# Optimization experiments

Hardware: AMD Instinct MI355X
Metric: run time of the kernel (lower is better)

## Reference

```python
import jax, jax.numpy as jnp
import numpy as np

N_NODES = 100000
N_EDGES = 1600000
IN_FEATS, HIDDEN_FEATS, OUT_FEATS = 32, 64, 16


def setup_inputs() -> dict:
    key = jax.random.key(0)
    ks = jax.random.split(key, 8)
    return {
        "features": jax.random.normal(ks[0], (N_NODES, IN_FEATS), dtype=jnp.float32),
        "src": jax.random.randint(ks[1], (N_EDGES,), 0, N_NODES, dtype=jnp.int64),
        "dst": jax.random.randint(ks[2], (N_EDGES,), 0, N_NODES, dtype=jnp.int64),
        "W1_self": jax.random.normal(ks[3], (IN_FEATS, HIDDEN_FEATS), dtype=jnp.float32) * 0.1,
        "W1_neigh": jax.random.normal(ks[4], (IN_FEATS, HIDDEN_FEATS), dtype=jnp.float32) * 0.1,
        "b1": jnp.zeros((HIDDEN_FEATS,), dtype=jnp.float32),
        "W2_self": jax.random.normal(ks[5], (HIDDEN_FEATS, OUT_FEATS), dtype=jnp.float32) * 0.1,
        "W2_neigh": jax.random.normal(ks[6], (HIDDEN_FEATS, OUT_FEATS), dtype=jnp.float32) * 0.1,
        "b2": jnp.zeros((OUT_FEATS,), dtype=jnp.float32),
    }


def _sage_conv_mean(h, src, dst, n_nodes, W_self, W_neigh, b):
    # DGL SAGEConv(mean): gather src features to edges, mean-reduce at dst,
    # then fc_self(h) + fc_neigh(mean_neigh) + bias.
    ones = jnp.ones(src.shape, dtype=h.dtype)
    deg = jax.ops.segment_sum(ones, dst, num_segments=n_nodes)  # in-degree [N]
    agg = jax.ops.segment_sum(h[src], dst, num_segments=n_nodes)  # [N, d]
    mean_neigh = agg / jnp.maximum(deg, 1.0)[:, None]
    return h @ W_self + mean_neigh @ W_neigh + b


def reference(features, src, dst, W1_self, W1_neigh, b1, W2_self, W2_neigh, b2):
    n = features.shape[0]
    h = _sage_conv_mean(features, src, dst, n, W1_self, W1_neigh, b1)
    h = jax.nn.relu(h)
    # dropout is identity at inference (Keras call default training=False)
    out = _sage_conv_mean(h, src, dst, n, W2_self, W2_neigh, b2)
    return out
```

## Files before the change

### kernel.cpp

```cpp
#include <hip/hip_runtime.h>

#define N_NODES 100000
#define N_EDGES 1600000
#define IN_F 32
#define HID_F 64
#define OUT_F 16
#define BSIZE 512
#define NBKT 256
#define CAP 10240
#define CHUNK 4096
#define NBUCK ((N_NODES + BSIZE - 1) / BSIZE)
#define APITCH 68

__device__ __forceinline__ unsigned f2bf(float f) {
  unsigned u = __float_as_uint(f);
  return (u + 0x7FFFu + ((u >> 16) & 1u)) >> 16;
}

#define ADD8(s, V) do { \
  s[0] += __uint_as_float((V).x << 16); \
  s[1] += __uint_as_float((V).x & 0xFFFF0000u); \
  s[2] += __uint_as_float((V).y << 16); \
  s[3] += __uint_as_float((V).y & 0xFFFF0000u); \
  s[4] += __uint_as_float((V).z << 16); \
  s[5] += __uint_as_float((V).z & 0xFFFF0000u); \
  s[6] += __uint_as_float((V).w << 16); \
  s[7] += __uint_as_float((V).w & 0xFFFF0000u); } while (0)

__global__ __launch_bounds__(256) void f2bf_kernel(
    const float4* __restrict__ in, uint4* __restrict__ outp) {
  int i = blockIdx.x * 256 + threadIdx.x;
  if (i >= N_NODES * IN_F / 8) return;
  float4 a = in[2 * i], b = in[2 * i + 1];
  uint4 r;
  r.x = f2bf(a.x) | (f2bf(a.y) << 16);
  r.y = f2bf(a.z) | (f2bf(a.w) << 16);
  r.z = f2bf(b.x) | (f2bf(b.y) << 16);
  r.w = f2bf(b.z) | (f2bf(b.w) << 16);
  outp[i] = r;
}

__global__ __launch_bounds__(NBKT) void cursor_init_kernel(int* __restrict__ cursor) {
  cursor[threadIdx.x] = threadIdx.x * CAP;
}

__global__ __launch_bounds__(512) void bucket_kernel(
    const int* __restrict__ src, const int* __restrict__ dst,
    int* __restrict__ cursor, unsigned* __restrict__ sorted) {
  __shared__ unsigned stage[CHUNK];
  __shared__ unsigned char sbkt[CHUNK];
  __shared__ int lcnt[NBKT], lscan[NBKT], gbase[NBKT];
  int t = threadIdx.x;
  if (t < NBKT) lcnt[t] = 0;
  __syncthreads();

  int base = blockIdx.x * CHUNK;
  unsigned mypk[CHUNK / 512];
  int myb[CHUNK / 512], myrank[CHUNK / 512];
#pragma unroll
  for (int i = 0; i < CHUNK / 512; ++i) {
    int e = base + t + 512 * i;
    if (e < N_EDGES) {
      unsigned s = (unsigned)src[e], d = (unsigned)dst[e];
      myb[i] = (int)(d >> 9);
      mypk[i] = (s << 9) | (d & 511u);
      myrank[i] = atomicAdd(&lcnt[myb[i]], 1);
    } else {
      myb[i] = -1;
    }
  }
  __syncthreads();
  if (t < NBKT) lscan[t] = lcnt[t];
  __syncthreads();
  for (int off = 1; off < NBKT; off <<= 1) {
    int v = (t < NBKT && t >= off) ? lscan[t - off] : 0;
    __syncthreads();
    if (t < NBKT) lscan[t] += v;
    __syncthreads();
  }
  if (t < NBKT) gbase[t] = lcnt[t] ? atomicAdd(&cursor[t], lcnt[t]) : 0;
  __syncthreads();
#pragma unroll
  for (int i = 0; i < CHUNK / 512; ++i) {
    if (myb[i] >= 0) {
      int slot = (lscan[myb[i]] - lcnt[myb[i]]) + myrank[i];
      stage[slot] = mypk[i];
      sbkt[slot] = (unsigned char)myb[i];
    }
  }
  __syncthreads();
  int nvalid = min(CHUNK, N_EDGES - base);
  for (int i = t; i < nvalid; i += 512) {
    unsigned p = stage[i];
    int b = (int)sbkt[i];
    int addr = gbase[b] + (i - (lscan[b] - lcnt[b]));
    sorted[addr] = p;
  }
}

__global__ __launch_bounds__(1024) void bcsr_kernel(
    const unsigned* __restrict__ sorted, const int* __restrict__ cursor,
    int* __restrict__ ptr, int* __restrict__ col) {
  __shared__ int lcnt[BSIZE];
  __shared__ int lcur[BSIZE];
  __shared__ int scanbuf[BSIZE];
  int t = threadIdx.x;
  int b = blockIdx.x;
  int base = b * CAP;
  int ne = cursor[b] - base;

  if (t < BSIZE) lcnt[t] = 0;
  __syncthreads();
  for (int i = t; i < ne; i += 1024)
    atomicAdd(&lcnt[sorted[base + i] & (BSIZE - 1)], 1);
  __syncthreads();

  int c = 0;
  if (t < BSIZE) { c = lcnt[t]; scanbuf[t] = c; }
  __syncthreads();
  for (int off = 1; off < BSIZE; off <<= 1) {
    int u = (t < BSIZE && t >= off) ? scanbuf[t - off] : 0;
    __syncthreads();
    if (t < BSIZE) scanbuf[t] += u;
    __syncthreads();
  }
  if (t < BSIZE) {
    int incl = scanbuf[t];
    lcur[t] = base + incl - c;
    int v = b * BSIZE + t;
    if (v < N_NODES) ptr[v] = base + incl;
  }
  __syncthreads();

  for (int i = t; i < ne; i += 1024) {
    unsigned p = sorted[base + i];
    int pos = atomicAdd(&lcur[p & (BSIZE - 1)], 1);
    col[pos] = (int)(p >> 9);
  }
}

__global__ __launch_bounds__(256) void gather1_kernel(
    const int* __restrict__ ptr, const int* __restrict__ col,
    const uint4* __restrict__ featbf, float* __restrict__ meanf) {
  int gid = blockIdx.x * 256 + threadIdx.x;
  int v = gid >> 2;
  int c = gid & 3;
  if (v >= N_NODES) return;
  int start = (v & (BSIZE - 1)) ? ptr[v - 1] : (v >> 9) * CAP;
  int end = ptr[v];
  float s[8] = {0.f, 0.f, 0.f, 0.f, 0.f, 0.f, 0.f, 0.f};
  int e = start;
  for (; e + 3 < end; e += 4) {
    uint4 q0 = featbf[col[e] * 4 + c];
    uint4 q1 = featbf[col[e + 1] * 4 + c];
    uint4 q2 = featbf[col[e + 2] * 4 + c];
    uint4 q3 = featbf[col[e + 3] * 4 + c];
    ADD8(s, q0);
    ADD8(s, q1);
    ADD8(s, q2);
    ADD8(s, q3);
  }
  for (; e < end; ++e) {
    uint4 q = featbf[col[e] * 4 + c];
    ADD8(s, q);
  }
  float inv = 1.0f / fmaxf((float)(end - start), 1.0f);
  float4 r0 = {s[0] * inv, s[1] * inv, s[2] * inv, s[3] * inv};
  float4 r1 = {s[4] * inv, s[5] * inv, s[6] * inv, s[7] * inv};
  ((float4*)meanf)[v * 8 + 2 * c] = r0;
  ((float4*)meanf)[v * 8 + 2 * c + 1] = r1;
}

__global__ __launch_bounds__(256) void l1t2s2_kernel(
    const float* __restrict__ feat, const float* __restrict__ meanf,
    const float* __restrict__ W1s, const float* __restrict__ W1n,
    const float* __restrict__ b1,
    const float* __restrict__ W2n, const float* __restrict__ W2s,
    unsigned* __restrict__ t2u, float* __restrict__ s2) {
  __shared__ float sA[64 * APITCH];
  __shared__ float sW[64 * 64];

  int t = threadIdx.x;
  int tile = blockIdx.x * 64;
  int nvalid = min(64, N_NODES - tile);

  {
    const float4* Fg = (const float4*)(feat + (size_t)tile * IN_F);
    const float4* Mg = (const float4*)(meanf + (size_t)tile * IN_F);
    int lim = nvalid * 8;
#pragma unroll
    for (int it = 0; it < 2; ++it) {
      int idx = t + 256 * it;
      int n = idx >> 3, c = idx & 7;
      if (idx < lim) {
        float4 a = Fg[idx];
        sA[(4 * c + 0) * APITCH + n] = a.x;
        sA[(4 * c + 1) * APITCH + n] = a.y;
        sA[(4 * c + 2) * APITCH + n] = a.z;
        sA[(4 * c + 3) * APITCH + n] = a.w;
        float4 m = Mg[idx];
        sA[(32 + 4 * c + 0) * APITCH + n] = m.x;
        sA[(32 + 4 * c + 1) * APITCH + n] = m.y;
        sA[(32 + 4 * c + 2) * APITCH + n] = m.z;
        sA[(32 + 4 * c + 3) * APITCH + n] = m.w;
      }
    }
  }
  {
    float4* Ws = (float4*)sW;
#pragma unroll
    for (int it = 0; it < 4; ++it) {
      int idx = t + 256 * it;
      int row = idx >> 4;
      const float4* srcw = (row < 32) ? (const float4*)W1s : (const float4*)W1n;
      Ws[idx] = srcw[(row & 31) * 16 + (idx & 15)];
    }
  }
  int tx = t & 15, ty = t >> 4;
  int n0 = 4 * ty, c0 = 4 * tx;
  float4 bb = ((const float4*)b1)[tx];
  __syncthreads();

  float acc[4][4];
#pragma unroll
  for (int i = 0; i < 4; ++i) { acc[i][0] = bb.x; acc[i][1] = bb.y; acc[i][2] = bb.z; acc[i][3] = bb.w; }
#pragma unroll 4
  for (int k = 0; k < 64; ++k) {
    float4 a = *(const float4*)&sA[k * APITCH + n0];
    float4 w = *(const float4*)&sW[k * 64 + c0];
    acc[0][0] += a.x * w.x; acc[0][1] += a.x * w.y; acc[0][2] += a.x * w.z; acc[0][3] += a.x * w.w;
    acc[1][0] += a.y * w.x; acc[1][1] += a.y * w.y; acc[1][2] += a.y * w.z; acc[1][3] += a.y * w.w;
    acc[2][0] += a.z * w.x; acc[2][1] += a.z * w.y; acc[2][2] += a.z * w.z; acc[2][3] += a.z * w.w;
    acc[3][0] += a.w * w.x; acc[3][1] += a.w * w.y; acc[3][2] += a.w * w.z; acc[3][3] += a.w * w.w;
  }
  __syncthreads();

#pragma unroll
  for (int jj = 0; jj < 4; ++jj) {
    float4 v;
    v.x = fmaxf(acc[0][jj], 0.0f);
    v.y = fmaxf(acc[1][jj], 0.0f);
    v.z = fmaxf(acc[2][jj], 0.0f);
    v.w = fmaxf(acc[3][jj], 0.0f);
    *(float4*)&sA[(c0 + jj) * APITCH + n0] = v;
  }
  {
    float4* Ws = (float4*)sW;
#pragma unroll
    for (int it = 0; it < 2; ++it) {
      int idx = t + 256 * it;
      int row = idx >> 3, ch = idx & 7;
      const float4* srcw = (ch < 4) ? (const float4*)W2n : (const float4*)W2s;
      Ws[row * 8 + ch] = srcw[row * 4 + (ch & 3)];
    }
  }
  __syncthreads();

  int c2 = 2 * tx;
  float a0 = 0.f, a1 = 0.f, b0 = 0.f, b1_ = 0.f, d0 = 0.f, d1 = 0.f, e0 = 0.f, e1 = 0.f;
#pragma unroll 4
  for (int k = 0; k < 64; ++k) {
    float4 a = *(const float4*)&sA[k * APITCH + n0];
    float2 w = *(const float2*)&sW[k * 32 + c2];
    a0 += a.x * w.x; a1 += a.x * w.y;
    b0 += a.y * w.x; b1_ += a.y * w.y;
    d0 += a.z * w.x; d1 += a.z * w.y;
    e0 += a.w * w.x; e1 += a.w * w.y;
  }
  {
    float rs[4][2] = {{a0, a1}, {b0, b1_}, {d0, d1}, {e0, e1}};
    int cc = c2 & 15;
#pragma unroll
    for (int i = 0; i < 4; ++i) {
      int v = tile + n0 + i;
      if (v < N_NODES) {
        if (c2 < 16) {
          t2u[v * 8 + (cc >> 1)] = f2bf(rs[i][0]) | (f2bf(rs[i][1]) << 16);
        } else {
          *(float2*)&s2[v * OUT_F + cc] = make_float2(rs[i][0], rs[i][1]);
        }
      }
    }
  }
}

__global__ __launch_bounds__(256) void gather2_final_kernel(
    const int* __restrict__ ptr, const int* __restrict__ col,
    const uint4* __restrict__ t2bf, const float* __restrict__ s2,
    const float* __restrict__ b2, float* __restrict__ out) {
  int gid = blockIdx.x * 256 + threadIdx.x;
  int v = gid >> 1;
  int c = gid & 1;
  if (v >= N_NODES) return;
  int start = (v & (BSIZE - 1)) ? ptr[v - 1] : (v >> 9) * CAP;
  int end = ptr[v];
  float s[8] = {0.f, 0.f, 0.f, 0.f, 0.f, 0.f, 0.f, 0.f};
  int e = start;
  for (; e + 3 < end; e += 4) {
    uint4 q0 = t2bf[col[e] * 2 + c];
    uint4 q1 = t2bf[col[e + 1] * 2 + c];
    uint4 q2 = t2bf[col[e + 2] * 2 + c];
    uint4 q3 = t2bf[col[e + 3] * 2 + c];
    ADD8(s, q0);
    ADD8(s, q1);
    ADD8(s, q2);
    ADD8(s, q3);
  }
  for (; e < end; ++e) {
    uint4 q = t2bf[col[e] * 2 + c];
    ADD8(s, q);
  }
  float inv = 1.0f / fmaxf((float)(end - start), 1.0f);
  float4 sv0 = ((const float4*)s2)[v * 4 + 2 * c];
  float4 sv1 = ((const float4*)s2)[v * 4 + 2 * c + 1];
  float4 bv0 = ((const float4*)b2)[2 * c];
  float4 bv1 = ((const float4*)b2)[2 * c + 1];
  float4 r0, r1;
  r0.x = sv0.x + bv0.x + s[0] * inv;
  r0.y = sv0.y + bv0.y + s[1] * inv;
  r0.z = sv0.z + bv0.z + s[2] * inv;
  r0.w = sv0.w + bv0.w + s[3] * inv;
  r1.x = sv1.x + bv1.x + s[4] * inv;
  r1.y = sv1.y + bv1.y + s[5] * inv;
  r1.z = sv1.z + bv1.z + s[6] * inv;
  r1.w = sv1.w + bv1.w + s[7] * inv;
  ((float4*)out)[v * 4 + 2 * c] = r0;
  ((float4*)out)[v * 4 + 2 * c + 1] = r1;
}

extern "C" void kernel_launch(void* const* d_in, const int* in_sizes, int n_in,
                              void* d_out, int out_size, void* d_ws, size_t ws_size,
                              hipStream_t stream) {
  const float* feat = (const float*)d_in[0];
  const int* src    = (const int*)d_in[1];
  const int* dst    = (const int*)d_in[2];
  const float* W1s  = (const float*)d_in[3];
  const float* W1n  = (const float*)d_in[4];
  const float* b1   = (const float*)d_in[5];
  const float* W2s  = (const float*)d_in[6];
  const float* W2n  = (const float*)d_in[7];
  const float* b2   = (const float*)d_in[8];
  float* out = (float*)d_out;

  const size_t N = N_NODES;
  const size_t SLAB = (size_t)NBKT * CAP;
  int* ptr = (int*)d_ws;
  int* col = ptr + N + 8;
  unsigned* sorted = (unsigned*)(col + SLAB);
  float* meanf = (float*)(sorted + SLAB);
  float* s2 = meanf + 32 * N;
  unsigned* featbf = (unsigned*)(s2 + 16 * N);
  unsigned* t2u = featbf + 16 * N;
  int* cursor = (int*)(t2u + 8 * N);

  f2bf_kernel<<<(N_NODES * IN_F / 8 + 255) / 256, 256, 0, stream>>>(
      (const float4*)feat, (uint4*)featbf);
  cursor_init_kernel<<<1, NBKT, 0, stream>>>(cursor);
  bucket_kernel<<<(N_EDGES + CHUNK - 1) / CHUNK, 512, 0, stream>>>(src, dst, cursor, sorted);
  bcsr_kernel<<<NBUCK, 1024, 0, stream>>>(sorted, cursor, ptr, col);

  gather1_kernel<<<(N_NODES * 4 + 255) / 256, 256, 0, stream>>>(
      ptr, col, (const uint4*)featbf, meanf);
  l1t2s2_kernel<<<(N_NODES + 63) / 64, 256, 0, stream>>>(feat, meanf, W1s, W1n, b1,
                                                         W2n, W2s, t2u, s2);
  gather2_final_kernel<<<(N_NODES * 2 + 255) / 256, 256, 0, stream>>>(
      ptr, col, (const uint4*)t2u, s2, b2, out);
}
```

Before: 190.4 us.

## Fuse layer-1 neighbor gather into transform kernel and fold cursor init

The layer-1 mean-aggregation gather now runs inside the layer-1 transform kernel and writes per-node means straight into the shared-memory A tile, so the fp32 meanf buffer is no longer written to and re-read from global memory. The cursor initialisation moves into block 0 of the bf16 conversion kernel, which removes one launch. The cost is that the fused kernel now has a long, degree-dependent gather phase before its GEMM, which could lower occupancy or load balance.

```diff
diff --git a/kernel.cpp b/kernel.cpp
--- a/kernel.cpp
+++ b/kernel.cpp
@@ -28,7 +28,9 @@
   s[7] += __uint_as_float((V).w & 0xFFFF0000u); } while (0)
 
 __global__ __launch_bounds__(256) void f2bf_kernel(
-    const float4* __restrict__ in, uint4* __restrict__ outp) {
+    const float4* __restrict__ in, uint4* __restrict__ outp,
+    int* __restrict__ cursor) {
+  if (blockIdx.x == 0) cursor[threadIdx.x] = threadIdx.x * CAP;
   int i = blockIdx.x * 256 + threadIdx.x;
   if (i >= N_NODES * IN_F / 8) return;
   float4 a = in[2 * i], b = in[2 * i + 1];
@@ -38,10 +40,6 @@
   r.z = f2bf(b.x) | (f2bf(b.y) << 16);
   r.w = f2bf(b.z) | (f2bf(b.w) << 16);
   outp[i] = r;
-}
-
-__global__ __launch_bounds__(NBKT) void cursor_init_kernel(int* __restrict__ cursor) {
-  cursor[threadIdx.x] = threadIdx.x * CAP;
 }
 
 __global__ __launch_bounds__(512) void bucket_kernel(
@@ -139,40 +137,9 @@
   }
 }
 
-__global__ __launch_bounds__(256) void gather1_kernel(
+__global__ __launch_bounds__(256) void l1g_kernel(
+    const float* __restrict__ feat, const uint4* __restrict__ featbf,
     const int* __restrict__ ptr, const int* __restrict__ col,
-    const uint4* __restrict__ featbf, float* __restrict__ meanf) {
-  int gid = blockIdx.x * 256 + threadIdx.x;
-  int v = gid >> 2;
-  int c = gid & 3;
-  if (v >= N_NODES) return;
-  int start = (v & (BSIZE - 1)) ? ptr[v - 1] : (v >> 9) * CAP;
-  int end = ptr[v];
-  float s[8] = {0.f, 0.f, 0.f, 0.f, 0.f, 0.f, 0.f, 0.f};
-  int e = start;
-  for (; e + 3 < end; e += 4) {
-    uint4 q0 = featbf[col[e] * 4 + c];
-    uint4 q1 = featbf[col[e + 1] * 4 + c];
-    uint4 q2 = featbf[col[e + 2] * 4 + c];
-    uint4 q3 = featbf[col[e + 3] * 4 + c];
-    ADD8(s, q0);
-    ADD8(s, q1);
-    ADD8(s, q2);
-    ADD8(s, q3);
-  }
-  for (; e < end; ++e) {
-    uint4 q = featbf[col[e] * 4 + c];
-    ADD8(s, q);
-  }
-  float inv = 1.0f / fmaxf((float)(end - start), 1.0f);
-  float4 r0 = {s[0] * inv, s[1] * inv, s[2] * inv, s[3] * inv};
-  float4 r1 = {s[4] * inv, s[5] * inv, s[6] * inv, s[7] * inv};
-  ((float4*)meanf)[v * 8 + 2 * c] = r0;
-  ((float4*)meanf)[v * 8 + 2 * c + 1] = r1;
-}
-
-__global__ __launch_bounds__(256) void l1t2s2_kernel(
-    const float* __restrict__ feat, const float* __restrict__ meanf,
     const float* __restrict__ W1s, const float* __restrict__ W1n,
     const float* __restrict__ b1,
     const float* __restrict__ W2n, const float* __restrict__ W2s,
@@ -185,8 +152,35 @@
   int nvalid = min(64, N_NODES - tile);
 
   {
+    int c = t & 3, nl = t >> 2;
+    int v = tile + nl;
+    if (nl < nvalid) {
+      int start = (v & (BSIZE - 1)) ? ptr[v - 1] : (v >> 9) * CAP;
+      int end = ptr[v];
+      float s[8] = {0.f, 0.f, 0.f, 0.f, 0.f, 0.f, 0.f, 0.f};
+      int e = start;
+      for (; e + 3 < end; e += 4) {
+        uint4 q0 = featbf[col[e] * 4 + c];
+        uint4 q1 = featbf[col[e + 1] * 4 + c];
+        uint4 q2 = featbf[col[e + 2] * 4 + c];
+        uint4 q3 = featbf[col[e + 3] * 4 + c];
+        ADD8(s, q0);
+        ADD8(s, q1);
+        ADD8(s, q2);
+        ADD8(s, q3);
+      }
+      for (; e < end; ++e) {
+        uint4 q = featbf[col[e] * 4 + c];
+        ADD8(s, q);
+      }
+      float inv = 1.0f / fmaxf((float)(end - start), 1.0f);
+#pragma unroll
+      for (int j = 0; j < 8; ++j)
+        sA[(32 + 8 * c + j) * APITCH + nl] = s[j] * inv;
+    }
+  }
+  {
     const float4* Fg = (const float4*)(feat + (size_t)tile * IN_F);
-    const float4* Mg = (const float4*)(meanf + (size_t)tile * IN_F);
     int lim = nvalid * 8;
 #pragma unroll
     for (int it = 0; it < 2; ++it) {
@@ -198,11 +192,6 @@
         sA[(4 * c + 1) * APITCH + n] = a.y;
         sA[(4 * c + 2) * APITCH + n] = a.z;
         sA[(4 * c + 3) * APITCH + n] = a.w;
-        float4 m = Mg[idx];
-        sA[(32 + 4 * c + 0) * APITCH + n] = m.x;
-        sA[(32 + 4 * c + 1) * APITCH + n] = m.y;
-        sA[(32 + 4 * c + 2) * APITCH + n] = m.z;
-        sA[(32 + 4 * c + 3) * APITCH + n] = m.w;
       }
     }
   }
@@ -347,22 +336,17 @@
   int* ptr = (int*)d_ws;
   int* col = ptr + N + 8;
   unsigned* sorted = (unsigned*)(col + SLAB);
-  float* meanf = (float*)(sorted + SLAB);
-  float* s2 = meanf + 32 * N;
+  float* s2 = (float*)(sorted + SLAB);
   unsigned* featbf = (unsigned*)(s2 + 16 * N);
   unsigned* t2u = featbf + 16 * N;
   int* cursor = (int*)(t2u + 8 * N);
 
   f2bf_kernel<<<(N_NODES * IN_F / 8 + 255) / 256, 256, 0, stream>>>(
-      (const float4*)feat, (uint4*)featbf);
-  cursor_init_kernel<<<1, NBKT, 0, stream>>>(cursor);
+      (const float4*)feat, (uint4*)featbf, cursor);
   bucket_kernel<<<(N_EDGES + CHUNK - 1) / CHUNK, 512, 0, stream>>>(src, dst, cursor, sorted);
   bcsr_kernel<<<NBUCK, 1024, 0, stream>>>(sorted, cursor, ptr, col);
-
-  gather1_kernel<<<(N_NODES * 4 + 255) / 256, 256, 0, stream>>>(
-      ptr, col, (const uint4*)featbf, meanf);
-  l1t2s2_kernel<<<(N_NODES + 63) / 64, 256, 0, stream>>>(feat, meanf, W1s, W1n, b1,
-                                                         W2n, W2s, t2u, s2);
+  l1g_kernel<<<(N_NODES + 63) / 64, 256, 0, stream>>>(
+      feat, (const uint4*)featbf, ptr, col, W1s, W1n, b1, W2n, W2s, t2u, s2);
   gather2_final_kernel<<<(N_NODES * 2 + 255) / 256, 256, 0, stream>>>(
       ptr, col, (const uint4*)t2u, s2, b2, out);
 }
```

Measured after the change: 179.2 us. 1.06x faster.
